# Kernel tuning notes

Hardware: AMD Instinct MI355X
Metric: run time of the kernel (lower is better)

Reference implementation:

```python
import jax, jax.numpy as jnp
import numpy as np
import math

EMBED_DIM = 1024
NUM_HEADS = 16
HEAD_DIM = EMBED_DIM // NUM_HEADS
INPUT_DIM = 1024


def setup_inputs() -> dict:
    key = jax.random.key(0)
    k_x, k_wqkv, k_wout = jax.random.split(key, 3)
    x = jax.random.normal(k_x, (4, 1, 2048, INPUT_DIM), dtype=jnp.float32)
    # xavier_uniform bounds
    def xavier(k, shape):
        fan_out, fan_in = shape
        bound = math.sqrt(6.0 / (fan_in + fan_out))
        return jax.random.uniform(k, shape, jnp.float32, -bound, bound)
    w_qkv = xavier(k_wqkv, (3 * EMBED_DIM, INPUT_DIM))
    b_qkv = jnp.zeros((3 * EMBED_DIM,), jnp.float32)
    w_out = xavier(k_wout, (EMBED_DIM, EMBED_DIM))
    b_out = jnp.zeros((EMBED_DIM,), jnp.float32)
    return {"x": x, "w_qkv": w_qkv, "b_qkv": b_qkv, "w_out": w_out, "b_out": b_out}


def reference(x, w_qkv, b_qkv, w_out, b_out):
    B, y, S, _ = x.shape  # y must be 1 (module reshape constraint)
    # QKV projection: [B, y, S, 3E]
    qkv = jnp.einsum('bysd,ed->byse', x, w_qkv) + b_qkv
    # reshape to [B, S, H, 3*head_dim] then [B, H, S, 3*head_dim]
    qkv = qkv.reshape(B, S, NUM_HEADS, 3 * HEAD_DIM).transpose(0, 2, 1, 3)
    q, k, v = jnp.split(qkv, 3, axis=-1)  # each [B, H, S, head_dim]
    logits = jnp.einsum('bhqd,bhkd->bhqk', q, k) / math.sqrt(HEAD_DIM)
    attn = jax.nn.softmax(logits, axis=-1)  # [B, H, S, S]
    vals = jnp.einsum('bhqk,bhkd->bhqd', attn, v)
    vals = vals.transpose(0, 2, 1, 3).reshape(B, S, EMBED_DIM)
    return jnp.einsum('bse,oe->bso', vals, w_out) + b_out  # [B, S, E]
```

## Files before the change

### kernel.cpp

```cpp
#include <hip/hip_runtime.h>

typedef __bf16 bf16;
typedef __bf16 bf16x8 __attribute__((ext_vector_type(8)));
typedef __bf16 bf16x4 __attribute__((ext_vector_type(4)));
typedef float f32x4 __attribute__((ext_vector_type(4)));
typedef float f32x16 __attribute__((ext_vector_type(16)));
typedef unsigned int u32x4 __attribute__((ext_vector_type(4)));

#define SM_SCALE 0.18033688011f

__device__ __forceinline__ f32x4 mfma16(bf16x8 a, bf16x8 b, f32x4 c) {
    return __builtin_amdgcn_mfma_f32_16x16x32_bf16(a, b, c, 0, 0, 0);
}
__device__ __forceinline__ f32x16 mfma32(bf16x8 a, bf16x8 b, f32x16 c) {
    return __builtin_amdgcn_mfma_f32_32x32x16_bf16(a, b, c, 0, 0, 0);
}

__device__ __forceinline__ void gload_lds16(const void* g, void* l) {
    __builtin_amdgcn_global_load_lds((const __attribute__((address_space(1))) void*)g,
                                     (__attribute__((address_space(3))) void*)l,
                                     16, 0, 0);
}

__device__ __forceinline__ unsigned cvtpk_bf16(float lo, float hi) {
    unsigned r;
    asm("v_cvt_pk_bf16_f32 %0, %1, %2" : "=v"(r) : "v"(lo), "v"(hi));
    return r;
}
__device__ __forceinline__ void plane32_swap(unsigned& a, unsigned& b) {
    asm("v_permlane32_swap_b32 %0, %1" : "+v"(a), "+v"(b));
}
__device__ __forceinline__ float vexp2(float x) {
    float r;
    asm("v_exp_f32 %0, %1" : "=v"(r) : "v"(x));
    return r;
}
__device__ __forceinline__ float vrcp(float x) {
    float r;
    asm("v_rcp_f32 %0, %1" : "=v"(r) : "v"(x));
    return r;
}

__device__ __forceinline__ void vpack_store(char* VwB, unsigned vwlow, bf16x8 v0, bf16x8 v1) {
    const u32x4 a = __builtin_bit_cast(u32x4, v0);
    const u32x4 b = __builtin_bit_cast(u32x4, v1);
#pragma unroll
    for (int j = 0; j < 8; ++j) {
        const unsigned sel = (j & 1) ? 0x07060302u : 0x05040100u;
        const unsigned w = __builtin_amdgcn_perm(b[j >> 1], a[j >> 1], sel);
        *(unsigned*)(VwB + j * 128 + (vwlow ^ (unsigned)(j << 4))) = w;
    }
}

__global__ void cvt_all(const float* __restrict__ x, const float* __restrict__ wq,
                        const float* __restrict__ wo, bf16* __restrict__ xb,
                        bf16* __restrict__ wqb, bf16* __restrict__ wob) {
    constexpr int NX = (8192 * 1024) / 4, NQ = (3072 * 1024) / 4, NO = (1024 * 1024) / 4;
    const int stride = gridDim.x * blockDim.x;
    for (int i = blockIdx.x * blockDim.x + threadIdx.x; i < NX + NQ + NO; i += stride) {
        const float* src;
        bf16* dst;
        int li;
        if (i < NX)           { src = x;  dst = xb;  li = i; }
        else if (i < NX + NQ) { src = wq; dst = wqb; li = i - NX; }
        else                  { src = wo; dst = wob; li = i - NX - NQ; }
        const f32x4 v = ((const f32x4*)src)[li];
        bf16x4 o;
#pragma unroll
        for (int j = 0; j < 4; ++j) o[j] = (bf16)v[j];
        ((bf16x4*)dst)[li] = o;
    }
}

#define G_TILE(BUF, STBUF, VM, DOSTAGE)                                     \
  {                                                                         \
    asm volatile("s_waitcnt vmcnt(" #VM ")" ::: "memory");                  \
    __builtin_amdgcn_s_barrier();                                           \
    bf16x8 af[4], bfr[4];                                                   \
    _Pragma("unroll") for (int mf = 0; mf < 4; ++mf)                        \
      af[mf] = *(const bf16x8*)(baseA[BUF] + mf * 1024);                    \
    _Pragma("unroll") for (int nf = 0; nf < 4; ++nf)                        \
      bfr[nf] = *(const bf16x8*)(baseB[BUF] + nf * 1024);                   \
    if (DOSTAGE) {                                                          \
      gload_lds16(apA0, ldA + (STBUF) * 16384);                             \
      gload_lds16(apA1, ldA + (STBUF) * 16384 + 4096);                      \
      gload_lds16(apB0, ldB + (STBUF) * 16384);                             \
      gload_lds16(apB1, ldB + (STBUF) * 16384 + 4096);                      \
      apA0 += 32; apA1 += 32; apB0 += 32; apB1 += 32;                       \
    }                                                                       \
    __builtin_amdgcn_s_setprio(1);                                          \
    _Pragma("unroll") for (int mf = 0; mf < 4; ++mf)                        \
      _Pragma("unroll") for (int nf = 0; nf < 4; ++nf)                      \
        acc[mf][nf] = mfma16(af[mf], bfr[nf], acc[mf][nf]);                 \
    __builtin_amdgcn_s_setprio(0);                                          \
  }

template <typename OutT, bool QSCALE>
__global__ __launch_bounds__(256) void gemm3d(const bf16* __restrict__ A,
                                              const bf16* __restrict__ Bw,
                                              const float* __restrict__ bias,
                                              OutT* __restrict__ C,
                                              int M, int N, int K) {
    __shared__ char lds[3 * 16384];
    const int tid = threadIdx.x;
    const int wave = tid >> 6, lane = tid & 63;
    const int ln15 = lane & 15, g4 = lane >> 4;
    const int wr = wave >> 1, wc = wave & 1;
    const int m0 = blockIdx.x * 128, n0 = blockIdx.y * 128;

    const int srow = lane >> 2;
    const int sgsw = ((lane & 3) ^ ((lane >> 2) & 3)) * 8;
    const bf16* apA0 = A  + (size_t)(m0 + wave * 16 + srow) * K + sgsw;
    const bf16* apA1 = A  + (size_t)(m0 + 64 + wave * 16 + srow) * K + sgsw;
    const bf16* apB0 = Bw + (size_t)(n0 + wave * 16 + srow) * K + sgsw;
    const bf16* apB1 = Bw + (size_t)(n0 + 64 + wave * 16 + srow) * K + sgsw;
    char* const ldA = (char*)lds + wave * 1024;
    char* const ldB = (char*)lds + 8192 + wave * 1024;

    const int kxr = (g4 * 16) ^ ((ln15 & 3) << 4);
    const char* baseA[3];
    const char* baseB[3];
#pragma unroll
    for (int b = 0; b < 3; ++b) {
        baseA[b] = (const char*)lds + b * 16384 + (wr * 64 + ln15) * 64 + kxr;
        baseB[b] = (const char*)lds + b * 16384 + 8192 + (wc * 64 + ln15) * 64 + kxr;
    }

    f32x4 acc[4][4] = {};

#pragma unroll
    for (int p = 0; p < 2; ++p) {
        gload_lds16(apA0, ldA + p * 16384);
        gload_lds16(apA1, ldA + p * 16384 + 4096);
        gload_lds16(apB0, ldB + p * 16384);
        gload_lds16(apB1, ldB + p * 16384 + 4096);
        apA0 += 32; apA1 += 32; apB0 += 32; apB1 += 32;
    }

    for (int g = 0; g < 10; ++g) {
        G_TILE(0, 2, 4, 1)
        G_TILE(1, 0, 4, 1)
        G_TILE(2, 1, 4, 1)
    }
    G_TILE(0, 0, 4, 0)
    G_TILE(1, 0, 0, 0)

    float bv[4], sc[4];
#pragma unroll
    for (int nj = 0; nj < 4; ++nj) {
        const int col = n0 + wc * 64 + nj * 16 + ln15;
        bv[nj] = bias[col];
        sc[nj] = (QSCALE && (col % 192) < 64) ? SM_SCALE : 1.0f;
    }
#pragma unroll
    for (int mi = 0; mi < 4; ++mi) {
#pragma unroll
        for (int nj = 0; nj < 4; ++nj) {
            const int col = n0 + wc * 64 + nj * 16 + ln15;
#pragma unroll
            for (int i = 0; i < 4; ++i) {
                const int row = m0 + wr * 64 + mi * 16 + g4 * 4 + i;
                C[(size_t)row * N + col] = (OutT)((acc[mi][nj][i] + bv[nj]) * sc[nj]);
            }
        }
    }
}

#define ATTN_ITER(CUR, PRE)                                                          \
  {                                                                                  \
    if (PRE) {                                                                       \
      gload_lds16(kp, (char*)Ks + ((CUR ^ 1) * 8192) + wave * 1024);                 \
      gload_lds16(kp + 32 * 3072, (char*)Ks + ((CUR ^ 1) * 8192) + (4 + wave) * 1024); \
      v0 = *(const bf16x8*)vp;                                                       \
      v1 = *(const bf16x8*)(vp + 3072);                                              \
      kp += 64 * 3072;                                                               \
      vp += 64 * 3072;                                                               \
    }                                                                                \
    _Pragma("unroll") for (int kh = 0; kh < 2; ++kh) {                               \
      f32x16 s;                                                                      \
      __builtin_amdgcn_s_setprio(1);                                                 \
      s = mfma32(*(const bf16x8*)(kra[0] + CUR * 8192 + kh * 4096), qf[0], z16);     \
      _Pragma("unroll") for (int dc = 1; dc < 4; ++dc) {                             \
        const bf16x8 kf = *(const bf16x8*)(kra[dc] + CUR * 8192 + kh * 4096);        \
        s = mfma32(kf, qf[dc], s);                                                   \
      }                                                                              \
      __builtin_amdgcn_s_setprio(0);                                                 \
      unsigned pk[8];                                                                \
      _Pragma("unroll") for (int m = 0; m < 8; ++m)                                  \
        pk[m] = cvtpk_bf16(vexp2(s[2 * m]), vexp2(s[2 * m + 1]));                    \
      plane32_swap(pk[0], pk[2]);                                                    \
      plane32_swap(pk[1], pk[3]);                                                    \
      plane32_swap(pk[4], pk[6]);                                                    \
      plane32_swap(pk[5], pk[7]);                                                    \
      const bf16x8 pf0 = __builtin_bit_cast(bf16x8, (u32x4){pk[0], pk[1], pk[2], pk[3]}); \
      const bf16x8 pf1 = __builtin_bit_cast(bf16x8, (u32x4){pk[4], pk[5], pk[6], pk[7]}); \
      __builtin_amdgcn_s_setprio(1);                                                 \
      {                                                                              \
        const bf16x8 va0 = *(const bf16x8*)(VsB + CUR * 8192 + (vroff0 ^ (kh * 64)));       \
        const bf16x8 vc0 = *(const bf16x8*)(VsB + CUR * 8192 + (vroff0 ^ (kh * 64 + 32)));  \
        o0 = mfma32(pf0, va0, o0);                                                   \
        o0 = mfma32(pf1, vc0, o0);                                                   \
        const bf16x8 va1 = *(const bf16x8*)(VsB + CUR * 8192 + (vroff1 ^ (kh * 64)));       \
        const bf16x8 vc1 = *(const bf16x8*)(VsB + CUR * 8192 + (vroff1 ^ (kh * 64 + 32)));  \
        o1 = mfma32(pf0, va1, o1);                                                   \
        o1 = mfma32(pf1, vc1, o1);                                                   \
        dsumC = mfma32(pf0, ones, dsumC);                                            \
        dsumC = mfma32(pf1, ones, dsumC);                                            \
      }                                                                              \
      __builtin_amdgcn_s_setprio(0);                                                 \
    }                                                                                \
    if (PRE) vpack_store((char*)Ks + 16384 + ((CUR ^ 1) * 8192) + vd8 * 128, vwlow, v0, v1); \
    __syncthreads();                                                                 \
  }

__global__ __launch_bounds__(256) void attn_fa(const bf16* __restrict__ qkv,
                                               bf16* __restrict__ vals) {
    const int b = blockIdx.x >> 4, h = blockIdx.x & 15;
    const int q0 = blockIdx.y * 128;
    const int tid = threadIdx.x, wave = tid >> 6, lane = tid & 63;
    const int ln31 = lane & 31, hi = lane >> 5;

    __shared__ bf16 Ks[2 * 4096 + 2 * 4096];

    const size_t base = ((size_t)b * 2048) * 3072 + (size_t)h * 192;
    const bf16* Qb = qkv + base;

    bf16x8 qf[4];
    {
        const size_t qr = (size_t)(q0 + wave * 32 + ln31) * 3072;
#pragma unroll
        for (int dc = 0; dc < 4; ++dc)
            qf[dc] = *(const bf16x8*)(Qb + qr + dc * 16 + hi * 8);
    }

    const int krow0 = wave * 8 + (lane >> 3);
    const int kgsw = ((lane & 7) ^ (lane >> 3)) * 8;
    const bf16* kp = qkv + base + 64 + (size_t)krow0 * 3072 + kgsw;
    const int vr2 = tid & 31, vd8 = (tid >> 5) * 8;
    const bf16* vp = qkv + base + 128 + (size_t)(2 * vr2) * 3072 + vd8;
    const unsigned vwlow = 4u * (unsigned)vr2;

    const int kxor = (ln31 & 7) << 4;
    const char* kra[4];
#pragma unroll
    for (int dc = 0; dc < 4; ++dc)
        kra[dc] = (char*)Ks + ln31 * 128 + ((dc * 32 + hi * 16) ^ kxor);
    const char* const VsB = (char*)Ks + 16384;
    const unsigned vroff0 = (unsigned)(ln31 * 128 + ((hi * 16) ^ kxor));
    const unsigned vroff1 = vroff0 + 32 * 128;

    const bf16x8 ones = __builtin_bit_cast(bf16x8, (u32x4){0x3F803F80u, 0x3F803F80u,
                                                           0x3F803F80u, 0x3F803F80u});
    const f32x16 z16 = {};
    f32x16 o0 = {}, o1 = {}, dsumC = {};
    bf16x8 v0, v1;

    gload_lds16(kp, (char*)Ks + wave * 1024);
    gload_lds16(kp + 32 * 3072, (char*)Ks + (4 + wave) * 1024);
    v0 = *(const bf16x8*)vp;
    v1 = *(const bf16x8*)(vp + 3072);
    kp += 64 * 3072;
    vp += 64 * 3072;
    vpack_store((char*)Ks + 16384 + vd8 * 128, vwlow, v0, v1);
    __syncthreads();

    for (int tp = 0; tp < 15; ++tp) {
        ATTN_ITER(0, true)
        ATTN_ITER(1, true)
    }
    ATTN_ITER(0, true)
    ATTN_ITER(1, false)

#pragma unroll
    for (int r = 0; r < 16; ++r) {
        const float invq = vrcp(dsumC[r]);
        const int qloc = (r & 3) + 8 * (r >> 2) + 4 * hi;
        const size_t orow = ((size_t)b * 2048 + q0 + wave * 32 + qloc) * 1024 + h * 64;
        vals[orow + ln31]      = (bf16)(o0[r] * invq);
        vals[orow + 32 + ln31] = (bf16)(o1[r] * invq);
    }
}

extern "C" void kernel_launch(void* const* d_in, const int* in_sizes, int n_in,
                              void* d_out, int out_size, void* d_ws, size_t ws_size,
                              hipStream_t stream) {
    const float* x     = (const float*)d_in[0];
    const float* w_qkv = (const float*)d_in[1];
    const float* b_qkv = (const float*)d_in[2];
    const float* w_out = (const float*)d_in[3];
    const float* b_out = (const float*)d_in[4];
    float* out = (float*)d_out;

    char* ws = (char*)d_ws;
    bf16* xb   = (bf16*)ws;
    bf16* wqb  = (bf16*)(ws + (16u << 20));
    bf16* wob  = (bf16*)(ws + (22u << 20));
    bf16* qkvb = (bf16*)(ws + (24u << 20));
    bf16* valb = xb;

    cvt_all<<<dim3(2048), dim3(256), 0, stream>>>(x, w_qkv, w_out, xb, wqb, wob);

    gemm3d<bf16, true><<<dim3(64, 24), dim3(256), 0, stream>>>(xb, wqb, b_qkv, qkvb,
                                                               8192, 3072, 1024);
    attn_fa<<<dim3(64, 16), dim3(256), 0, stream>>>(qkvb, valb);
    gemm3d<float, false><<<dim3(64, 8), dim3(256), 0, stream>>>(valb, wob, b_out, out,
                                                                8192, 1024, 1024);
}
```

Baseline: 191.1 us.

## Enlarge GEMM tiles to 256x128 with 8 waves and 64-wide K stages

Replaces the 128x128, 4-wave GEMM with a 256x128 tile computed by 8 waves. Each pipeline stage now loads a 64-wide K slice into a triple-buffered LDS ring with an 8-way XOR swizzle, and each stage issues two MFMA sub-steps. The goal is to double reuse of the weight tile, halve the number of barriers per K, and raise MFMA density in both projection GEMMs. In exchange it uses 144KB of LDS per block, which limits occupancy to one block per CU. The output-projection grid also drops to 256 blocks, which may underfill the CUs.

```diff
diff --git a/kernel.cpp b/kernel.cpp
--- a/kernel.cpp
+++ b/kernel.cpp
@@ -72,78 +72,82 @@
     }
 }
 
-#define G_TILE(BUF, STBUF, VM, DOSTAGE)                                     \
+#define G_STAGE(STBUF)                                                      \
+    gload_lds16(apA,             ldsA + (STBUF) * 49152);                   \
+    gload_lds16(apA +  8 * 1024, ldsA + (STBUF) * 49152 + 1024);            \
+    gload_lds16(apA + 16 * 1024, ldsA + (STBUF) * 49152 + 2048);            \
+    gload_lds16(apA + 24 * 1024, ldsA + (STBUF) * 49152 + 3072);            \
+    gload_lds16(apB,             ldsB + (STBUF) * 49152);                   \
+    gload_lds16(apB +  8 * 1024, ldsB + (STBUF) * 49152 + 1024);            \
+    apA += 64; apB += 64;
+
+#define G_TILE(BUF, VM, STBUF, DOSTAGE)                                     \
   {                                                                         \
     asm volatile("s_waitcnt vmcnt(" #VM ")" ::: "memory");                  \
     __builtin_amdgcn_s_barrier();                                           \
-    bf16x8 af[4], bfr[4];                                                   \
+    bf16x8 a0[4], b0[4];                                                    \
     _Pragma("unroll") for (int mf = 0; mf < 4; ++mf)                        \
-      af[mf] = *(const bf16x8*)(baseA[BUF] + mf * 1024);                    \
+      a0[mf] = *(const bf16x8*)(baseAk0 + (BUF) * 49152 + mf * 2048);       \
     _Pragma("unroll") for (int nf = 0; nf < 4; ++nf)                        \
-      bfr[nf] = *(const bf16x8*)(baseB[BUF] + nf * 1024);                   \
-    if (DOSTAGE) {                                                          \
-      gload_lds16(apA0, ldA + (STBUF) * 16384);                             \
-      gload_lds16(apA1, ldA + (STBUF) * 16384 + 4096);                      \
-      gload_lds16(apB0, ldB + (STBUF) * 16384);                             \
-      gload_lds16(apB1, ldB + (STBUF) * 16384 + 4096);                      \
-      apA0 += 32; apA1 += 32; apB0 += 32; apB1 += 32;                       \
-    }                                                                       \
+      b0[nf] = *(const bf16x8*)(baseBk0 + (BUF) * 49152 + nf * 2048);       \
+    if (DOSTAGE) { G_STAGE(STBUF) }                                         \
     __builtin_amdgcn_s_setprio(1);                                          \
     _Pragma("unroll") for (int mf = 0; mf < 4; ++mf)                        \
       _Pragma("unroll") for (int nf = 0; nf < 4; ++nf)                      \
-        acc[mf][nf] = mfma16(af[mf], bfr[nf], acc[mf][nf]);                 \
+        acc[mf][nf] = mfma16(a0[mf], b0[nf], acc[mf][nf]);                  \
+    __builtin_amdgcn_s_setprio(0);                                          \
+    bf16x8 a1[4], b1[4];                                                    \
+    _Pragma("unroll") for (int mf = 0; mf < 4; ++mf)                        \
+      a1[mf] = *(const bf16x8*)(baseAk1 + (BUF) * 49152 + mf * 2048);       \
+    _Pragma("unroll") for (int nf = 0; nf < 4; ++nf)                        \
+      b1[nf] = *(const bf16x8*)(baseBk1 + (BUF) * 49152 + nf * 2048);       \
+    __builtin_amdgcn_s_setprio(1);                                          \
+    _Pragma("unroll") for (int mf = 0; mf < 4; ++mf)                        \
+      _Pragma("unroll") for (int nf = 0; nf < 4; ++nf)                      \
+        acc[mf][nf] = mfma16(a1[mf], b1[nf], acc[mf][nf]);                  \
     __builtin_amdgcn_s_setprio(0);                                          \
   }
 
 template <typename OutT, bool QSCALE>
-__global__ __launch_bounds__(256) void gemm3d(const bf16* __restrict__ A,
-                                              const bf16* __restrict__ Bw,
-                                              const float* __restrict__ bias,
-                                              OutT* __restrict__ C,
-                                              int M, int N, int K) {
-    __shared__ char lds[3 * 16384];
+__global__ __launch_bounds__(512) void gemm256(const bf16* __restrict__ A,
+                                               const bf16* __restrict__ Bw,
+                                               const float* __restrict__ bias,
+                                               OutT* __restrict__ C,
+                                               int M, int N, int K) {
+    __shared__ char lds[3 * 49152];
     const int tid = threadIdx.x;
     const int wave = tid >> 6, lane = tid & 63;
     const int ln15 = lane & 15, g4 = lane >> 4;
     const int wr = wave >> 1, wc = wave & 1;
-    const int m0 = blockIdx.x * 128, n0 = blockIdx.y * 128;
-
-    const int srow = lane >> 2;
-    const int sgsw = ((lane & 3) ^ ((lane >> 2) & 3)) * 8;
-    const bf16* apA0 = A  + (size_t)(m0 + wave * 16 + srow) * K + sgsw;
-    const bf16* apA1 = A  + (size_t)(m0 + 64 + wave * 16 + srow) * K + sgsw;
-    const bf16* apB0 = Bw + (size_t)(n0 + wave * 16 + srow) * K + sgsw;
-    const bf16* apB1 = Bw + (size_t)(n0 + 64 + wave * 16 + srow) * K + sgsw;
-    char* const ldA = (char*)lds + wave * 1024;
-    char* const ldB = (char*)lds + 8192 + wave * 1024;
-
-    const int kxr = (g4 * 16) ^ ((ln15 & 3) << 4);
-    const char* baseA[3];
-    const char* baseB[3];
-#pragma unroll
-    for (int b = 0; b < 3; ++b) {
-        baseA[b] = (const char*)lds + b * 16384 + (wr * 64 + ln15) * 64 + kxr;
-        baseB[b] = (const char*)lds + b * 16384 + 8192 + (wc * 64 + ln15) * 64 + kxr;
-    }
+    const int m0 = blockIdx.x * 256, n0 = blockIdx.y * 128;
+
+    const int srow = lane >> 3;
+    const int sgsw = ((lane & 7) ^ srow) * 8;
+    const bf16* apA = A  + (size_t)(m0 + wave * 32 + srow) * K + sgsw;
+    const bf16* apB = Bw + (size_t)(n0 + wave * 16 + srow) * K + sgsw;
+    char* const ldsA = (char*)lds + wave * 4096;
+    char* const ldsB = (char*)lds + 32768 + wave * 2048;
+
+    const int cxor = ((g4 ^ (ln15 & 7)) << 4);
+    const char* baseAk0 = (const char*)lds + (wr * 64 + ln15) * 128 + cxor;
+    const char* baseAk1 = (const char*)lds + (((wr * 64 + ln15) * 128 + cxor) ^ 64);
+    const char* baseBk0 = (const char*)lds + 32768 + (wc * 64 + ln15) * 128 + cxor;
+    const char* baseBk1 = (const char*)lds + 32768 + (((wc * 64 + ln15) * 128 + cxor) ^ 64);
 
     f32x4 acc[4][4] = {};
 
-#pragma unroll
-    for (int p = 0; p < 2; ++p) {
-        gload_lds16(apA0, ldA + p * 16384);
-        gload_lds16(apA1, ldA + p * 16384 + 4096);
-        gload_lds16(apB0, ldB + p * 16384);
-        gload_lds16(apB1, ldB + p * 16384 + 4096);
-        apA0 += 32; apA1 += 32; apB0 += 32; apB1 += 32;
-    }
-
-    for (int g = 0; g < 10; ++g) {
-        G_TILE(0, 2, 4, 1)
-        G_TILE(1, 0, 4, 1)
-        G_TILE(2, 1, 4, 1)
-    }
-    G_TILE(0, 0, 4, 0)
-    G_TILE(1, 0, 0, 0)
+    G_STAGE(0)
+    G_STAGE(1)
+
+    for (int g = 0; g < 4; ++g) {
+        G_TILE(0, 6, 2, 1)
+        G_TILE(1, 6, 0, 1)
+        G_TILE(2, 6, 1, 1)
+    }
+    G_TILE(0, 6, 2, 1)
+    G_TILE(1, 6, 0, 1)
+    G_TILE(2, 6, 0, 0)
+    G_TILE(0, 0, 0, 0)
 
     float bv[4], sc[4];
 #pragma unroll
@@ -300,9 +304,9 @@
 
     cvt_all<<<dim3(2048), dim3(256), 0, stream>>>(x, w_qkv, w_out, xb, wqb, wob);
 
-    gemm3d<bf16, true><<<dim3(64, 24), dim3(256), 0, stream>>>(xb, wqb, b_qkv, qkvb,
-                                                               8192, 3072, 1024);
+    gemm256<bf16, true><<<dim3(32, 24), dim3(512), 0, stream>>>(xb, wqb, b_qkv, qkvb,
+                                                                8192, 3072, 1024);
     attn_fa<<<dim3(64, 16), dim3(256), 0, stream>>>(qkvb, valb);
-    gemm3d<float, false><<<dim3(64, 8), dim3(256), 0, stream>>>(valb, wob, b_out, out,
-                                                                8192, 1024, 1024);
-}
+    gemm256<float, false><<<dim3(32, 8), dim3(512), 0, stream>>>(valb, wob, b_out, out,
+                                                                 8192, 1024, 1024);
+}
```

New measurement: 186.7 us, median of 4. 1.02x faster.
